# Performance work log

Measured on AMD Instinct MI355X. Metric: run time of the kernel, lower is better.

The kernel has to match this reference:

```python
import jax, jax.numpy as jnp
import numpy as np

B, D_IN, D_H, D_OUT, E = 4096, 1024, 4096, 1024, 8
N_ACTIVE = 5              # max(1, int(8 * 0.625))
TEMP = float(np.e)        # BoltzmannGate default temperature
N_CAMP_A = E // 2


def setup_inputs() -> dict:
    key = jax.random.key(0)
    ks = jax.random.split(key, 6)
    s_in = 1.0 / np.sqrt(D_IN)
    s_h = 1.0 / np.sqrt(D_H)
    return {
        "x": jax.random.normal(ks[0], (B, D_IN), jnp.float32),
        "gate_w": jax.random.normal(ks[1], (D_IN, E), jnp.float32) * s_in,
        "gate_b": jnp.zeros((E,), jnp.float32),
        "w1": jax.random.normal(ks[2], (E, D_IN, D_H), jnp.float32) * s_in,
        "b1": jnp.zeros((E, D_H), jnp.float32),
        "w2": jax.random.normal(ks[3], (E, D_H, D_OUT), jnp.float32) * s_h,
        "b2": jnp.zeros((E, D_OUT), jnp.float32),
        "ph_alpha": jnp.array(1.0, jnp.float32),
        "ph_beta": jnp.array(0.0, jnp.float32),
    }


def _forward(x, gate_w, gate_b, w1, b1, w2, b2, ph_alpha, ph_beta):
    # BoltzmannGate: softmax over temperature-scaled scores, top-k mask, renorm
    scores = (x @ gate_w + gate_b) / TEMP                 # [B, E]
    probs = jax.nn.softmax(scores, axis=-1)
    _, topk_idx = jax.lax.top_k(probs, N_ACTIVE)          # [B, k]
    rows = jnp.arange(x.shape[0])[:, None]
    mask = jnp.zeros_like(probs).at[rows, topk_idx].set(1.0)
    w = probs * mask
    weights = w / (w.sum(axis=-1, keepdims=True) + 1e-8)  # [B, E]

    # Dense evaluation of all experts (dropout is inference-mode identity)
    h = jax.nn.relu(jnp.einsum("bi,eih->beh", x, w1) + b1)     # [B, E, H]
    e_out = jnp.einsum("beh,eho->beo", h, w2) + b2             # [B, E, O]

    # Camp A = experts [0, E//2), Camp G = experts [E//2, E)
    out_a = jnp.einsum("be,beo->bo", weights[:, :N_CAMP_A], e_out[:, :N_CAMP_A])
    out_g = jnp.einsum("be,beo->bo", weights[:, N_CAMP_A:], e_out[:, N_CAMP_A:])

    repulsion = out_a - out_g
    # PH distance proxy computed on detached tensors in torch -> stop_gradient
    diff = jax.lax.stop_gradient(repulsion)
    l2 = jnp.linalg.norm(diff, axis=-1)                   # [B]
    var = jnp.var(diff, axis=-1)                          # population var, ddof=0
    ph_dist = l2 * (1.0 + var)
    ph_corr = jax.nn.sigmoid(ph_alpha * ph_dist + ph_beta) * 2.0  # in (0, 2)
    output = repulsion * ph_corr[:, None]
    return output, out_a, out_g


def reference(x, gate_w, gate_b, w1, b1, w2, b2, ph_alpha, ph_beta):
    return _forward(x, gate_w, gate_b, w1, b1, w2, b2, ph_alpha, ph_beta)
```

## Files before the change

### kernel.cpp

```cpp
#include <hip/hip_runtime.h>
#include <hip/hip_bf16.h>
#include <stdint.h>

typedef unsigned short u16;
typedef unsigned int u32;
typedef __attribute__((ext_vector_type(4))) float f32x4;
typedef __attribute__((ext_vector_type(4))) int i32x4;
typedef __attribute__((ext_vector_type(8))) u16 u16x8;
typedef __attribute__((ext_vector_type(8))) __bf16 bf16x8;

constexpr int BATCH = 4096, DIN = 1024, DH = 4096, DOUT = 1024, NEXP = 8;
constexpr int HS_CAP = 2816;

struct Ptr4 { float* p[4]; };

__device__ __forceinline__ u16 f2bf(float f) {
  u32 u = __float_as_uint(f);
  u += 0x7fffu + ((u >> 16) & 1u);
  return (u16)(u >> 16);
}

#define GLOAD_LDS16(gp, lp)                                                    \
  __builtin_amdgcn_global_load_lds(                                           \
      (__attribute__((address_space(1))) void*)(gp),                          \
      (__attribute__((address_space(3))) void*)(lp), 16, 0, 0)

#define BAR()                                                                  \
  { asm volatile("" ::: "memory"); __builtin_amdgcn_s_barrier();               \
    asm volatile("" ::: "memory"); }
#define VM4() asm volatile("s_waitcnt vmcnt(4)" ::: "memory")
#define VM0() asm volatile("s_waitcnt vmcnt(0)" ::: "memory")

#define STG4(q0, q1, kofs, dst)                                                \
  { GLOAD_LDS16((q0) + (kofs), (dst));                                         \
    GLOAD_LDS16((q1) + (kofs), (dst) + 4096); }

__global__ void gate_kernel(const float* __restrict__ x,
                            const float* __restrict__ gw,
                            const float* __restrict__ gb,
                            float* __restrict__ wgt) {
  const int wave = threadIdx.x >> 6, lane = threadIdx.x & 63;
  const int b = blockIdx.x * 4 + wave;
  const float* xr = x + (size_t)b * DIN;
  float acc[NEXP];
#pragma unroll
  for (int e = 0; e < NEXP; ++e) acc[e] = 0.f;
  for (int k = lane; k < DIN; k += 64) {
    const float xv = xr[k];
    const f32x4 g0 = *(const f32x4*)(gw + (size_t)k * NEXP);
    const f32x4 g1 = *(const f32x4*)(gw + (size_t)k * NEXP + 4);
    acc[0] += xv * g0[0]; acc[1] += xv * g0[1];
    acc[2] += xv * g0[2]; acc[3] += xv * g0[3];
    acc[4] += xv * g1[0]; acc[5] += xv * g1[1];
    acc[6] += xv * g1[2]; acc[7] += xv * g1[3];
  }
#pragma unroll
  for (int off = 32; off; off >>= 1)
#pragma unroll
    for (int e = 0; e < NEXP; ++e) acc[e] += __shfl_xor(acc[e], off);
  if (lane == 0) {
    const float invT = 0.36787944117144233f;
    float s[NEXP], mx = -1e30f;
    for (int e = 0; e < NEXP; ++e) { s[e] = (acc[e] + gb[e]) * invT; mx = fmaxf(mx, s[e]); }
    float p[NEXP], sum = 0.f;
    for (int e = 0; e < NEXP; ++e) { p[e] = expf(s[e] - mx); sum += p[e]; }
    const float inv = 1.f / sum;
    for (int e = 0; e < NEXP; ++e) p[e] *= inv;
    float w[NEXP], wsum = 0.f;
    for (int e = 0; e < NEXP; ++e) {
      int cnt = 0;
      for (int j = 0; j < NEXP; ++j) cnt += (p[j] > p[e]) || (p[j] == p[e] && j < e);
      w[e] = (cnt < 5) ? p[e] : 0.f;
      wsum += w[e];
    }
    const float inv2 = 1.f / (wsum + 1e-8f);
    for (int e = 0; e < NEXP; ++e) wgt[(size_t)b * NEXP + e] = w[e] * inv2;
  }
}

__global__ void assign_kernel(const float* __restrict__ wgt,
                              int* __restrict__ cnt, u16* __restrict__ ridx) {
  const int b = blockIdx.x * 256 + threadIdx.x;
#pragma unroll
  for (int e = 0; e < NEXP; ++e) {
    if (wgt[(size_t)b * NEXP + e] != 0.f) {
      const int pos = atomicAdd(&cnt[e], 1);
      if (pos < BATCH) ridx[e * BATCH + pos] = (u16)b;
    }
  }
}

__global__ void build_items(const int* __restrict__ cnt,
                            u32* __restrict__ items, int* __restrict__ itot) {
  if (threadIdx.x != 0) return;
  int t = 0;
  for (int e = 0; e < NEXP; ++e) {
    int c = cnt[e]; c = c < HS_CAP ? c : HS_CAP;
    const int nm = (c + 255) >> 8;
    for (int n = 0; n < DH / 256; ++n)
      for (int m = 0; m < nm; ++m)
        items[t++] = ((u32)e << 12) | ((u32)n << 6) | (u32)m;
  }
  itot[0] = t;
}

__global__ void gather_cvt(const float* __restrict__ x,
                           const int* __restrict__ cnt,
                           const u16* __restrict__ ridx,
                           u16* __restrict__ Xe) {
  const int e = blockIdx.y, p = blockIdx.x;
  int c = cnt[e]; c = c < HS_CAP ? c : HS_CAP;
  if (p >= c) return;
  const int row = ridx[e * BATCH + p];
  const float* s = x + (size_t)row * DIN;
  u16* d = Xe + ((size_t)e * HS_CAP + p) * DIN;
  const int t = threadIdx.x;
  const f32x4 a = *(const f32x4*)(s + t * 8);
  const f32x4 b = *(const f32x4*)(s + t * 8 + 4);
  u16x8 o;
  o[0] = f2bf(a[0]); o[1] = f2bf(a[1]); o[2] = f2bf(a[2]); o[3] = f2bf(a[3]);
  o[4] = f2bf(b[0]); o[5] = f2bf(b[1]); o[6] = f2bf(b[2]); o[7] = f2bf(b[3]);
  *(u16x8*)(d + t * 8) = o;
}

__global__ void transpose_cvt(const float* __restrict__ src, u16* __restrict__ dst,
                              int C, int ldd, size_t src_slice,
                              size_t dst_hi, size_t dst_lo) {
  __shared__ float ts[64][65];
  const int z = blockIdx.z;
  const float* s = src + (size_t)z * src_slice;
  u16* d = dst + (size_t)(z >> 2) * dst_hi + (size_t)(z & 3) * dst_lo;
  const int c0 = blockIdx.x * 64, r0 = blockIdx.y * 64;
  const int t = threadIdx.x;
  const int lr = t >> 4, lc = (t & 15) * 4;
#pragma unroll
  for (int i = 0; i < 4; ++i) {
    const f32x4 v = *(const f32x4*)(s + (size_t)(r0 + i * 16 + lr) * C + c0 + lc);
    ts[i * 16 + lr][lc] = v[0];
    ts[i * 16 + lr][lc + 1] = v[1];
    ts[i * 16 + lr][lc + 2] = v[2];
    ts[i * 16 + lr][lc + 3] = v[3];
  }
  __syncthreads();
  const int cc = t >> 3, r8 = (t & 7) * 8;
#pragma unroll
  for (int pass = 0; pass < 2; ++pass) {
    const int c = cc + pass * 32;
    u16x8 o;
#pragma unroll
    for (int j = 0; j < 8; ++j) o[j] = f2bf(ts[r8 + j][c]);
    *(u16x8*)(d + (size_t)(c0 + c) * ldd + r0 + r8) = o;
  }
}

__device__ __forceinline__ void rdB4(i32x4 rB[2][2], const char* base, int wc,
                                     int roff, int NH) {
#pragma unroll
  for (int n = 0; n < 2; ++n)
#pragma unroll
    for (int kk = 0; kk < 2; ++kk)
      rB[n][kk] = *(const i32x4*)(base + (((wc * 4 + NH * 2 + n) * 2 + kk) << 10) + roff);
}
template <int MH>
__device__ __forceinline__ void rdA8(i32x4 rA[4][2], const char* base, int wr, int roff) {
#pragma unroll
  for (int m = 0; m < 4; ++m)
#pragma unroll
    for (int kk = 0; kk < 2; ++kk)
      rA[m][kk] = *(const i32x4*)(base + (((wr * 8 + MH * 4 + m) * 2 + kk) << 10) + roff);
}
template <int MH, int NH>
__device__ __forceinline__ void mm16(f32x4 acc[8][4], const i32x4 rA[4][2],
                                     const i32x4 rB[2][2]) {
  __builtin_amdgcn_s_setprio(1);
#pragma unroll
  for (int m = 0; m < 4; ++m)
#pragma unroll
    for (int n = 0; n < 2; ++n)
#pragma unroll
      for (int kk = 0; kk < 2; ++kk)
        acc[MH * 4 + m][NH * 2 + n] = __builtin_amdgcn_mfma_f32_16x16x32_bf16(
            __builtin_bit_cast(bf16x8, rA[m][kk]),
            __builtin_bit_cast(bf16x8, rB[n][kk]),
            acc[MH * 4 + m][NH * 2 + n], 0, 0, 0);
  __builtin_amdgcn_s_setprio(0);
}

#define TILE_BODY(T, CA, CB_, DA_OT, DB_CB)                                    \
  {                                                                            \
    const int t_ = (T);                                                        \
    const bool g1 = (t_ + 1) < NT, g2 = (t_ + 2) < NT;                         \
    const int kA = (t_ + 1) * 64, kB = (t_ + 2) * 64;                          \
    rdA8<0>(rA, CA, wr, roff);                                                 \
    rdB4(rB0, CB_, wc, roff, 0);                                               \
    if (g1) STG4(qA0, qA1, kA, DA_OT);                                         \
    BAR();                                                                     \
    mm16<0, 0>(acc, rA, rB0);                                                  \
    BAR();                                                                     \
    rdB4(rB1, CB_, wc, roff, 1);                                               \
    if (g1) STG4(qA2, qA3, kA, DA_OT + 8192);                                  \
    BAR();                                                                     \
    mm16<0, 1>(acc, rA, rB1);                                                  \
    BAR();                                                                     \
    rdA8<1>(rA, CA, wr, roff);                                                 \
    if (g2) STG4(qB0, qB1, kB, DB_CB);                                         \
    BAR();                                                                     \
    mm16<1, 1>(acc, rA, rB1);                                                  \
    BAR();                                                                     \
    if (g2) {                                                                  \
      STG4(qB2, qB3, kB, DB_CB + 8192);                                        \
      BAR();                                                                   \
      mm16<1, 0>(acc, rA, rB0);                                                \
      VM4();                                                                   \
    } else {                                                                   \
      BAR();                                                                   \
      mm16<1, 0>(acc, rA, rB0);                                                \
      VM0();                                                                   \
    }                                                                          \
    BAR();                                                                     \
  }

__global__ __launch_bounds__(512, 2) void gemm256p(
    const u16* __restrict__ Xe, const u16* __restrict__ w1t,
    u16* __restrict__ Hs, const float* __restrict__ wgt,
    const float* __restrict__ b1,
    const int* __restrict__ cnt, const u16* __restrict__ ridx,
    const int* __restrict__ itot, const u32* __restrict__ items) {
  __shared__ __align__(16) u16 sA[2][16384];
  __shared__ __align__(16) u16 sB[2][16384];

  const int tid = threadIdx.x;
  const int w = tid >> 6, lane = tid & 63;
  const int l15 = lane & 15, lh = lane >> 4;
  const int wr = w >> 2, wc = w & 3;

  const int lp = lane ^ ((lane & 32) >> 4);
  const int grow = (w >> 1) * 16 + (lp >> 2);
  const int gcol = (w & 1) * 32 + (lp & 3) * 8;
  const int roff = l15 * 64 + ((lh * 16) ^ ((l15 & 8) << 2));
  const char* cA0 = (const char*)&sA[0][0];
  const char* cA1 = (const char*)&sA[1][0];
  const char* cB0 = (const char*)&sB[0][0];
  const char* cB1 = (const char*)&sB[1][0];
  u16* dA0 = &sA[0][w * 512];
  u16* dA1 = &sA[1][w * 512];
  u16* dB0 = &sB[0][w * 512];
  u16* dB1 = &sB[1][w * 512];

  const int total = itot[0];
  const int lo = (int)(((long)blockIdx.x * total) >> 8);
  const int hi = (int)((((long)blockIdx.x + 1) * total) >> 8);
  constexpr int NT = DIN / 64;

  for (int ii = lo; ii < hi; ++ii) {
    const u32 it = items[ii];
    const int e = it >> 12, n = (it >> 6) & 63, m = it & 63;
    const int bM = m * 256, bN = n * 256;
    int count = cnt[e]; count = count < HS_CAP ? count : HS_CAP;
    const int eoff = e * BATCH;

    const u16* A = Xe + (size_t)e * HS_CAP * DIN;
    const u16* Bt = w1t + (size_t)e * DH * DIN;
    const float* bias = b1 + (size_t)e * DH;
    u16* dstH = Hs + (size_t)e * HS_CAP * DH;

    const u16* qA0 = A + (size_t)(bM + grow) * DIN + gcol;
    const u16* qA1 = qA0 + (size_t)64 * DIN;
    const u16* qA2 = qA0 + (size_t)128 * DIN;
    const u16* qA3 = qA0 + (size_t)192 * DIN;
    const u16* qB0 = Bt + (size_t)(bN + grow) * DIN + gcol;
    const u16* qB1 = qB0 + (size_t)64 * DIN;
    const u16* qB2 = qB0 + (size_t)128 * DIN;
    const u16* qB3 = qB0 + (size_t)192 * DIN;

    f32x4 acc[8][4] = {};
    i32x4 rA[4][2], rB0[2][2], rB1[2][2];

    STG4(qB0, qB1, 0, dB0);
    STG4(qB2, qB3, 0, dB0 + 8192);
    STG4(qA0, qA1, 0, dA0);
    STG4(qA2, qA3, 0, dA0 + 8192);
    STG4(qB0, qB1, 64, dB1);
    STG4(qB2, qB3, 64, dB1 + 8192);
    VM4();
    BAR();

    for (int t = 0; t < NT; t += 2) {
      TILE_BODY(t, cA0, cB0, dA1, dB0);
      TILE_BODY(t + 1, cA1, cB1, dA0, dB1);
    }

#pragma unroll
    for (int m2 = 0; m2 < 8; ++m2)
#pragma unroll
      for (int r = 0; r < 4; ++r) {
        const int pos = bM + wr * 128 + m2 * 16 + lh * 4 + r;
        if (pos >= count) continue;
        const int orow = ridx[eoff + pos];
        const float wsc = wgt[(size_t)orow * NEXP + e];
#pragma unroll
        for (int nn = 0; nn < 4; ++nn) {
          const int col = bN + wc * 64 + nn * 16 + l15;
          float v = acc[m2][nn][r] + bias[col];
          v = fmaxf(v, 0.0f) * wsc;
          dstH[(size_t)pos * DH + col] = f2bf(v);
        }
      }
  }
}

template <int EPI>
__global__ __launch_bounds__(512, 2) void gemm256(
    const u16* __restrict__ A0, int lda,
    const u16* __restrict__ Bt0, int ldb, int K,
    u16* __restrict__ dstH0, Ptr4 parts,
    const float* __restrict__ wgt, const float* __restrict__ bias0,
    const int* __restrict__ cnt, const u16* __restrict__ ridx, int camp,
    int NM, int NN) {
  __shared__ __align__(16) u16 sA[2][16384];
  __shared__ __align__(16) u16 sB[2][16384];

  const int tid = threadIdx.x;
  const int w = tid >> 6, lane = tid & 63;
  const int l15 = lane & 15, lh = lane >> 4;
  const int wr = w >> 2, wc = w & 3;

  const int cpx = (int)gridDim.x >> 3;
  const int id = blockIdx.x;
  const int wk = (id & 7) * cpx + (id >> 3);
  const int m = wk % NM;
  const int n = (wk / NM) % NN;
  const int z = wk / (NM * NN);
  const int bM = m * 256, bN = n * 256;

  const int expert = camp * 4 + z;
  int count = cnt[expert];
  count = count < HS_CAP ? count : HS_CAP;
  if (bM >= count) return;
  const int eoff = expert * BATCH;

  const u16* A;
  const u16* Bt;
  const float* bias = bias0;
  u16* dstH = dstH0;
  if (EPI == 0) {
    A = A0 + (size_t)expert * HS_CAP * lda;
    Bt = Bt0 + (size_t)expert * DH * DIN;
    bias = bias0 + (size_t)expert * DH;
    dstH = dstH0 + (size_t)z * HS_CAP * DH;
  } else {
    A = A0 + (size_t)z * HS_CAP * lda;
    Bt = Bt0 + (size_t)z * DH;
  }

  const int lp = lane ^ ((lane & 32) >> 4);
  const int grow = (w >> 1) * 16 + (lp >> 2);
  const int gcol = (w & 1) * 32 + (lp & 3) * 8;

  const u16* qA0 = A + (size_t)(bM + grow) * lda + gcol;
  const u16* qA1 = qA0 + (size_t)64 * lda;
  const u16* qA2 = qA0 + (size_t)128 * lda;
  const u16* qA3 = qA0 + (size_t)192 * lda;
  const u16* qB0 = Bt + (size_t)(bN + grow) * ldb + gcol;
  const u16* qB1 = qB0 + (size_t)64 * ldb;
  const u16* qB2 = qB0 + (size_t)128 * ldb;
  const u16* qB3 = qB0 + (size_t)192 * ldb;

  u16* dA0 = &sA[0][w * 512];
  u16* dA1 = &sA[1][w * 512];
  u16* dB0 = &sB[0][w * 512];
  u16* dB1 = &sB[1][w * 512];

  const int roff = l15 * 64 + ((lh * 16) ^ ((l15 & 8) << 2));
  const char* cA0 = (const char*)&sA[0][0];
  const char* cA1 = (const char*)&sA[1][0];
  const char* cB0 = (const char*)&sB[0][0];
  const char* cB1 = (const char*)&sB[1][0];

  const int NT = K >> 6;
  f32x4 acc[8][4] = {};
  i32x4 rA[4][2], rB0[2][2], rB1[2][2];

  STG4(qB0, qB1, 0, dB0);
  STG4(qB2, qB3, 0, dB0 + 8192);
  STG4(qA0, qA1, 0, dA0);
  STG4(qA2, qA3, 0, dA0 + 8192);
  STG4(qB0, qB1, 64, dB1);
  STG4(qB2, qB3, 64, dB1 + 8192);
  VM4();
  BAR();

  for (int t = 0; t < NT; t += 2) {
    TILE_BODY(t, cA0, cB0, dA1, dB0);
    TILE_BODY(t + 1, cA1, cB1, dA0, dB1);
  }

  if (EPI == 0) {
#pragma unroll
    for (int m2 = 0; m2 < 8; ++m2)
#pragma unroll
      for (int r = 0; r < 4; ++r) {
        const int pos = bM + wr * 128 + m2 * 16 + lh * 4 + r;
        if (pos >= count) continue;
        const int orow = ridx[eoff + pos];
        const float wsc = wgt[(size_t)orow * NEXP + expert];
#pragma unroll
        for (int nn = 0; nn < 4; ++nn) {
          const int col = bN + wc * 64 + nn * 16 + l15;
          float v = acc[m2][nn][r] + bias[col];
          v = fmaxf(v, 0.0f) * wsc;
          dstH[(size_t)pos * DH + col] = f2bf(v);
        }
      }
  } else {
    float* __restrict__ P = parts.p[z];
#pragma unroll
    for (int m2 = 0; m2 < 8; ++m2)
#pragma unroll
      for (int r = 0; r < 4; ++r) {
        const int pos = bM + wr * 128 + m2 * 16 + lh * 4 + r;
        if (pos >= count) continue;
        const int orow = ridx[eoff + pos];
#pragma unroll
        for (int nn = 0; nn < 4; ++nn) {
          const int col = bN + wc * 64 + nn * 16 + l15;
          P[(size_t)orow * DOUT + col] = acc[m2][nn][r];
        }
      }
  }
}

__global__ void reduce_kernel(float* __restrict__ dst,
                              const float* __restrict__ p0, const float* __restrict__ p1,
                              const float* __restrict__ p2, const float* __restrict__ p3,
                              const float* __restrict__ wgt,
                              const float* __restrict__ b2c, int camp) {
  const int b = blockIdx.x, t = threadIdx.x;
  const f32x4 wv = *(const f32x4*)(wgt + (size_t)b * NEXP + camp * 4);
  const size_t ro = (size_t)b * DOUT;
#pragma unroll
  for (int j = 0; j < 4; ++j) {
    const int i = j * 256 + t;
    float acc = wv[0] * b2c[i] + wv[1] * b2c[DOUT + i] +
                wv[2] * b2c[2 * DOUT + i] + wv[3] * b2c[3 * DOUT + i];
    acc += (wv[0] != 0.f) ? p0[ro + i] : 0.f;
    acc += (wv[1] != 0.f) ? p1[ro + i] : 0.f;
    acc += (wv[2] != 0.f) ? p2[ro + i] : 0.f;
    acc += (wv[3] != 0.f) ? p3[ro + i] : 0.f;
    dst[ro + i] = acc;
  }
}

__global__ void final_kernel(float* __restrict__ out,
                             const float* __restrict__ alpha,
                             const float* __restrict__ beta) {
  const int b = blockIdx.x, t = threadIdx.x;
  const float* pa = out + (size_t)BATCH * DOUT + (size_t)b * DOUT;
  const float* pg = out + (size_t)2 * BATCH * DOUT + (size_t)b * DOUT;
  float* po = out + (size_t)b * DOUT;
  float d[4], s1 = 0.f, s2 = 0.f;
#pragma unroll
  for (int j = 0; j < 4; ++j) {
    const int i = j * 256 + t;
    d[j] = pa[i] - pg[i];
    s1 += d[j];
    s2 += d[j] * d[j];
  }
#pragma unroll
  for (int off = 32; off; off >>= 1) {
    s1 += __shfl_xor(s1, off);
    s2 += __shfl_xor(s2, off);
  }
  __shared__ float r1[4], r2[4];
  if ((t & 63) == 0) { r1[t >> 6] = s1; r2[t >> 6] = s2; }
  __syncthreads();
  s1 = r1[0] + r1[1] + r1[2] + r1[3];
  s2 = r2[0] + r2[1] + r2[2] + r2[3];
  const float mean = s1 * (1.f / DOUT);
  const float var = s2 * (1.f / DOUT) - mean * mean;
  const float dist = sqrtf(s2) * (1.f + var);
  const float zz = alpha[0] * dist + beta[0];
  const float corr = 2.f / (1.f + expf(-zz));
#pragma unroll
  for (int j = 0; j < 4; ++j) po[j * 256 + t] = d[j] * corr;
}

extern "C" void kernel_launch(void* const* d_in, const int* in_sizes, int n_in,
                              void* d_out, int out_size, void* d_ws, size_t ws_size,
                              hipStream_t stream) {
  const float* x   = (const float*)d_in[0];
  const float* gw  = (const float*)d_in[1];
  const float* gb  = (const float*)d_in[2];
  const float* w1  = (const float*)d_in[3];
  const float* b1  = (const float*)d_in[4];
  const float* w2  = (const float*)d_in[5];
  const float* b2  = (const float*)d_in[6];
  const float* pha = (const float*)d_in[7];
  const float* phb = (const float*)d_in[8];
  float* out = (float*)d_out;
  float* out_a = out + (size_t)BATCH * DOUT;
  float* out_g = out + (size_t)2 * BATCH * DOUT;

  char* ws = (char*)d_ws;
  float* wgt  = (float*)ws;
  int* cnt    = (int*)(ws + 131072);
  u16* ridx   = (u16*)(ws + 135168);
  u32* items  = (u32*)(ws + 200704);
  int* itot   = (int*)(ws + 258048);
  u16* Xe     = (u16*)(ws + 262144);
  constexpr size_t XE_BYTES  = (size_t)NEXP * HS_CAP * DIN * 2;
  constexpr size_t W1T_BYTES = (size_t)NEXP * DH * DIN * 2;
  constexpr size_t W2T_BYTES = (size_t)DOUT * 4 * DH * 2;
  constexpr size_t P_BYTES   = (size_t)BATCH * DOUT * 4;
  constexpr size_t HS_E      = (size_t)HS_CAP * DH * 2;
  const size_t w1t_off = 262144 + XE_BYTES;
  u16* w1t = (u16*)(ws + w1t_off);

  const size_t merged_need = w1t_off + W1T_BYTES + 2 * P_BYTES + 8 * HS_E;
  const bool merged = (ws_size >= merged_need);

  constexpr int NM = HS_CAP / 256;
  constexpr int NN1 = DH / 256, NN2 = DOUT / 256;

  gate_kernel<<<BATCH / 4, 256, 0, stream>>>(x, gw, gb, wgt);
  hipMemsetAsync(cnt, 0, NEXP * sizeof(int), stream);
  assign_kernel<<<BATCH / 256, 256, 0, stream>>>(wgt, cnt, ridx);
  build_items<<<1, 64, 0, stream>>>(cnt, items, itot);
  gather_cvt<<<dim3(HS_CAP, NEXP), 128, 0, stream>>>(x, cnt, ridx, Xe);
  transpose_cvt<<<dim3(DH / 64, DIN / 64, NEXP), 256, 0, stream>>>(
      w1, w1t, DH, DIN, (size_t)DIN * DH, (size_t)4 * DH * DIN, (size_t)DH * DIN);

  if (merged) {
    float* P0 = (float*)(ws + w1t_off + W1T_BYTES);
    float* P1 = (float*)(ws + w1t_off + W1T_BYTES + P_BYTES);
    u16* Hs   = (u16*)(ws + w1t_off + W1T_BYTES + 2 * P_BYTES);
    u16* w2t0 = w1t;
    u16* w2t1 = (u16*)((char*)w1t + W2T_BYTES);
    Ptr4 pc0 = {{out_a, out, out_g, P0}};
    Ptr4 pc1 = {{out_g, out, P0, P1}};

    gemm256p<<<256, 512, 0, stream>>>(Xe, w1t, Hs, wgt, b1, cnt, ridx, itot, items);
    transpose_cvt<<<dim3(DOUT / 64, DH / 64, 4), 256, 0, stream>>>(
        w2, w2t0, DOUT, 4 * DH, (size_t)DH * DOUT, 0, (size_t)DH);
    transpose_cvt<<<dim3(DOUT / 64, DH / 64, 4), 256, 0, stream>>>(
        w2 + (size_t)4 * DH * DOUT, w2t1, DOUT, 4 * DH, (size_t)DH * DOUT, 0, (size_t)DH);

    gemm256<2><<<NM * NN2 * 4, 512, 0, stream>>>(
        Hs, DH, w2t0, 4 * DH, DH, nullptr, pc0, nullptr, nullptr, cnt, ridx, 0, NM, NN2);
    reduce_kernel<<<BATCH, 256, 0, stream>>>(out_a, out_a, out, out_g, P0, wgt, b2, 0);
    gemm256<2><<<NM * NN2 * 4, 512, 0, stream>>>(
        Hs + (size_t)4 * HS_CAP * DH, DH, w2t1, 4 * DH, DH, nullptr, pc1,
        nullptr, nullptr, cnt, ridx, 1, NM, NN2);
    reduce_kernel<<<BATCH, 256, 0, stream>>>(out_g, out_g, out, P0, P1, wgt,
                                             b2 + (size_t)4 * DOUT, 1);
  } else {
    u16* w2t1 = w1t;
    u16* w2t0 = (u16*)(ws + w1t_off + W1T_BYTES);
    float* P0 = (float*)(ws + w1t_off + W1T_BYTES + W2T_BYTES);
    float* P1 = (float*)(ws + w1t_off + W1T_BYTES + W2T_BYTES + P_BYTES);
    u16* Hs   = (u16*)(ws + w1t_off + W1T_BYTES + W2T_BYTES + 2 * P_BYTES);
    Ptr4 pc0 = {{out_a, out, out_g, P0}};
    Ptr4 pc1 = {{out_g, out, P0, P1}};

    transpose_cvt<<<dim3(DOUT / 64, DH / 64, 4), 256, 0, stream>>>(
        w2, w2t0, DOUT, 4 * DH, (size_t)DH * DOUT, 0, (size_t)DH);
    gemm256<0><<<NM * NN1 * 4, 512, 0, stream>>>(
        Xe, DIN, w1t, DIN, DIN, Hs, pc0, wgt, b1, cnt, ridx, 0, NM, NN1);
    transpose_cvt<<<dim3(DOUT / 64, DH / 64, 4), 256, 0, stream>>>(
        w2 + (size_t)4 * DH * DOUT, w2t1, DOUT, 4 * DH, (size_t)DH * DOUT, 0, (size_t)DH);
    gemm256<2><<<NM * NN2 * 4, 512, 0, stream>>>(
        Hs, DH, w2t0, 4 * DH, DH, nullptr, pc0, nullptr, nullptr, cnt, ridx, 0, NM, NN2);
    reduce_kernel<<<BATCH, 256, 0, stream>>>(out_a, out_a, out, out_g, P0, wgt, b2, 0);
    gemm256<0><<<NM * NN1 * 4, 512, 0, stream>>>(
        Xe, DIN, w1t, DIN, DIN, Hs, pc1, wgt, b1, cnt, ridx, 1, NM, NN1);
    gemm256<2><<<NM * NN2 * 4, 512, 0, stream>>>(
        Hs, DH, w2t1, 4 * DH, DH, nullptr, pc1, nullptr, nullptr, cnt, ridx, 1, NM, NN2);
    reduce_kernel<<<BATCH, 256, 0, stream>>>(out_g, out_g, out, P0, P1, wgt,
                                             b2 + (size_t)4 * DOUT, 1);
  }

  final_kernel<<<BATCH, 256, 0, stream>>>(out, pha, phb);
}
```

Measured before the change: 728.3 us.

## Overlap camp-A layer-2 GEMM with camp-G layer-1 GEMM in one combo launch

Removes the persistent item-list GEMM and its build_items kernel. When the workspace is large enough, w2 is transposed into separate buffers up front. The camp-A layer-1 GEMM then runs, followed by a single combined launch whose blocks run either the camp-A layer-2 GEMM or the camp-G layer-1 GEMM, so the two overlap on the device. The last reduce is also fused into the final PH-correction kernel, removing one pass over the output. The cost is a larger workspace requirement and a heterogeneous grid whose tiles may be unevenly balanced.

```diff
diff --git a/kernel.cpp b/kernel.cpp
--- a/kernel.cpp
+++ b/kernel.cpp
@@ -88,20 +88,6 @@
       if (pos < BATCH) ridx[e * BATCH + pos] = (u16)b;
     }
   }
-}
-
-__global__ void build_items(const int* __restrict__ cnt,
-                            u32* __restrict__ items, int* __restrict__ itot) {
-  if (threadIdx.x != 0) return;
-  int t = 0;
-  for (int e = 0; e < NEXP; ++e) {
-    int c = cnt[e]; c = c < HS_CAP ? c : HS_CAP;
-    const int nm = (c + 255) >> 8;
-    for (int n = 0; n < DH / 256; ++n)
-      for (int m = 0; m < nm; ++m)
-        items[t++] = ((u32)e << 12) | ((u32)n << 6) | (u32)m;
-  }
-  itot[0] = t;
 }
 
 __global__ void gather_cvt(const float* __restrict__ x,
@@ -220,95 +206,6 @@
     BAR();                                                                     \
   }
 
-__global__ __launch_bounds__(512, 2) void gemm256p(
-    const u16* __restrict__ Xe, const u16* __restrict__ w1t,
-    u16* __restrict__ Hs, const float* __restrict__ wgt,
-    const float* __restrict__ b1,
-    const int* __restrict__ cnt, const u16* __restrict__ ridx,
-    const int* __restrict__ itot, const u32* __restrict__ items) {
-  __shared__ __align__(16) u16 sA[2][16384];
-  __shared__ __align__(16) u16 sB[2][16384];
-
-  const int tid = threadIdx.x;
-  const int w = tid >> 6, lane = tid & 63;
-  const int l15 = lane & 15, lh = lane >> 4;
-  const int wr = w >> 2, wc = w & 3;
-
-  const int lp = lane ^ ((lane & 32) >> 4);
-  const int grow = (w >> 1) * 16 + (lp >> 2);
-  const int gcol = (w & 1) * 32 + (lp & 3) * 8;
-  const int roff = l15 * 64 + ((lh * 16) ^ ((l15 & 8) << 2));
-  const char* cA0 = (const char*)&sA[0][0];
-  const char* cA1 = (const char*)&sA[1][0];
-  const char* cB0 = (const char*)&sB[0][0];
-  const char* cB1 = (const char*)&sB[1][0];
-  u16* dA0 = &sA[0][w * 512];
-  u16* dA1 = &sA[1][w * 512];
-  u16* dB0 = &sB[0][w * 512];
-  u16* dB1 = &sB[1][w * 512];
-
-  const int total = itot[0];
-  const int lo = (int)(((long)blockIdx.x * total) >> 8);
-  const int hi = (int)((((long)blockIdx.x + 1) * total) >> 8);
-  constexpr int NT = DIN / 64;
-
-  for (int ii = lo; ii < hi; ++ii) {
-    const u32 it = items[ii];
-    const int e = it >> 12, n = (it >> 6) & 63, m = it & 63;
-    const int bM = m * 256, bN = n * 256;
-    int count = cnt[e]; count = count < HS_CAP ? count : HS_CAP;
-    const int eoff = e * BATCH;
-
-    const u16* A = Xe + (size_t)e * HS_CAP * DIN;
-    const u16* Bt = w1t + (size_t)e * DH * DIN;
-    const float* bias = b1 + (size_t)e * DH;
-    u16* dstH = Hs + (size_t)e * HS_CAP * DH;
-
-    const u16* qA0 = A + (size_t)(bM + grow) * DIN + gcol;
-    const u16* qA1 = qA0 + (size_t)64 * DIN;
-    const u16* qA2 = qA0 + (size_t)128 * DIN;
-    const u16* qA3 = qA0 + (size_t)192 * DIN;
-    const u16* qB0 = Bt + (size_t)(bN + grow) * DIN + gcol;
-    const u16* qB1 = qB0 + (size_t)64 * DIN;
-    const u16* qB2 = qB0 + (size_t)128 * DIN;
-    const u16* qB3 = qB0 + (size_t)192 * DIN;
-
-    f32x4 acc[8][4] = {};
-    i32x4 rA[4][2], rB0[2][2], rB1[2][2];
-
-    STG4(qB0, qB1, 0, dB0);
-    STG4(qB2, qB3, 0, dB0 + 8192);
-    STG4(qA0, qA1, 0, dA0);
-    STG4(qA2, qA3, 0, dA0 + 8192);
-    STG4(qB0, qB1, 64, dB1);
-    STG4(qB2, qB3, 64, dB1 + 8192);
-    VM4();
-    BAR();
-
-    for (int t = 0; t < NT; t += 2) {
-      TILE_BODY(t, cA0, cB0, dA1, dB0);
-      TILE_BODY(t + 1, cA1, cB1, dA0, dB1);
-    }
-
-#pragma unroll
-    for (int m2 = 0; m2 < 8; ++m2)
-#pragma unroll
-      for (int r = 0; r < 4; ++r) {
-        const int pos = bM + wr * 128 + m2 * 16 + lh * 4 + r;
-        if (pos >= count) continue;
-        const int orow = ridx[eoff + pos];
-        const float wsc = wgt[(size_t)orow * NEXP + e];
-#pragma unroll
-        for (int nn = 0; nn < 4; ++nn) {
-          const int col = bN + wc * 64 + nn * 16 + l15;
-          float v = acc[m2][nn][r] + bias[col];
-          v = fmaxf(v, 0.0f) * wsc;
-          dstH[(size_t)pos * DH + col] = f2bf(v);
-        }
-      }
-  }
-}
-
 template <int EPI>
 __global__ __launch_bounds__(512, 2) void gemm256(
     const u16* __restrict__ A0, int lda,
@@ -430,6 +327,131 @@
   }
 }
 
+__global__ __launch_bounds__(512, 2) void gemm_combo(
+    const u16* __restrict__ Hs0, const u16* __restrict__ w2t0, Ptr4 pc0,
+    const u16* __restrict__ Xe, const u16* __restrict__ w1t,
+    u16* __restrict__ HsW, const float* __restrict__ b1,
+    const float* __restrict__ wgt,
+    const int* __restrict__ cnt, const u16* __restrict__ ridx, int l2n) {
+  __shared__ __align__(16) u16 sA[2][16384];
+  __shared__ __align__(16) u16 sB[2][16384];
+
+  const int tid = threadIdx.x;
+  const int w = tid >> 6, lane = tid & 63;
+  const int l15 = lane & 15, lh = lane >> 4;
+  const int wr = w >> 2, wc = w & 3;
+
+  const bool isL2 = (int)blockIdx.x < l2n;
+  const int id = isL2 ? (int)blockIdx.x : (int)blockIdx.x - l2n;
+  const int tot = isL2 ? l2n : ((int)gridDim.x - l2n);
+  const int cpx = tot >> 3;
+  const int wk = (id & 7) * cpx + (id >> 3);
+  const int NM = HS_CAP / 256;
+  const int NN = isL2 ? (DOUT / 256) : (DH / 256);
+  const int m = wk % NM;
+  const int n = (wk / NM) % NN;
+  const int z = wk / (NM * NN);
+  const int bM = m * 256, bN = n * 256;
+
+  const int expert = isL2 ? z : 4 + z;
+  int count = cnt[expert];
+  count = count < HS_CAP ? count : HS_CAP;
+  if (bM >= count) return;
+  const int eoff = expert * BATCH;
+
+  const u16* A; const u16* Bt;
+  int lda, ldb, K;
+  const float* bias = nullptr;
+  u16* dstH = nullptr;
+  if (isL2) {
+    A = Hs0 + (size_t)z * HS_CAP * DH;  lda = DH;
+    Bt = w2t0 + (size_t)z * DH;         ldb = 4 * DH;
+    K = DH;
+  } else {
+    A = Xe + (size_t)expert * HS_CAP * DIN;  lda = DIN;
+    Bt = w1t + (size_t)expert * DH * DIN;    ldb = DIN;
+    K = DIN;
+    bias = b1 + (size_t)expert * DH;
+    dstH = HsW + (size_t)expert * HS_CAP * DH;
+  }
+
+  const int lp = lane ^ ((lane & 32) >> 4);
+  const int grow = (w >> 1) * 16 + (lp >> 2);
+  const int gcol = (w & 1) * 32 + (lp & 3) * 8;
+
+  const u16* qA0 = A + (size_t)(bM + grow) * lda + gcol;
+  const u16* qA1 = qA0 + (size_t)64 * lda;
+  const u16* qA2 = qA0 + (size_t)128 * lda;
+  const u16* qA3 = qA0 + (size_t)192 * lda;
+  const u16* qB0 = Bt + (size_t)(bN + grow) * ldb + gcol;
+  const u16* qB1 = qB0 + (size_t)64 * ldb;
+  const u16* qB2 = qB0 + (size_t)128 * ldb;
+  const u16* qB3 = qB0 + (size_t)192 * ldb;
+
+  u16* dA0 = &sA[0][w * 512];
+  u16* dA1 = &sA[1][w * 512];
+  u16* dB0 = &sB[0][w * 512];
+  u16* dB1 = &sB[1][w * 512];
+
+  const int roff = l15 * 64 + ((lh * 16) ^ ((l15 & 8) << 2));
+  const char* cA0 = (const char*)&sA[0][0];
+  const char* cA1 = (const char*)&sA[1][0];
+  const char* cB0 = (const char*)&sB[0][0];
+  const char* cB1 = (const char*)&sB[1][0];
+
+  const int NT = K >> 6;
+  f32x4 acc[8][4] = {};
+  i32x4 rA[4][2], rB0[2][2], rB1[2][2];
+
+  STG4(qB0, qB1, 0, dB0);
+  STG4(qB2, qB3, 0, dB0 + 8192);
+  STG4(qA0, qA1, 0, dA0);
+  STG4(qA2, qA3, 0, dA0 + 8192);
+  STG4(qB0, qB1, 64, dB1);
+  STG4(qB2, qB3, 64, dB1 + 8192);
+  VM4();
+  BAR();
+
+  for (int t = 0; t < NT; t += 2) {
+    TILE_BODY(t, cA0, cB0, dA1, dB0);
+    TILE_BODY(t + 1, cA1, cB1, dA0, dB1);
+  }
+
+  if (isL2) {
+    float* __restrict__ P = pc0.p[z];
+#pragma unroll
+    for (int m2 = 0; m2 < 8; ++m2)
+#pragma unroll
+      for (int r = 0; r < 4; ++r) {
+        const int pos = bM + wr * 128 + m2 * 16 + lh * 4 + r;
+        if (pos >= count) continue;
+        const int orow = ridx[eoff + pos];
+#pragma unroll
+        for (int nn = 0; nn < 4; ++nn) {
+          const int col = bN + wc * 64 + nn * 16 + l15;
+          P[(size_t)orow * DOUT + col] = acc[m2][nn][r];
+        }
+      }
+  } else {
+#pragma unroll
+    for (int m2 = 0; m2 < 8; ++m2)
+#pragma unroll
+      for (int r = 0; r < 4; ++r) {
+        const int pos = bM + wr * 128 + m2 * 16 + lh * 4 + r;
+        if (pos >= count) continue;
+        const int orow = ridx[eoff + pos];
+        const float wsc = wgt[(size_t)orow * NEXP + expert];
+#pragma unroll
+        for (int nn = 0; nn < 4; ++nn) {
+          const int col = bN + wc * 64 + nn * 16 + l15;
+          float v = acc[m2][nn][r] + bias[col];
+          v = fmaxf(v, 0.0f) * wsc;
+          dstH[(size_t)pos * DH + col] = f2bf(v);
+        }
+      }
+  }
+}
+
 __global__ void reduce_kernel(float* __restrict__ dst,
                               const float* __restrict__ p0, const float* __restrict__ p1,
                               const float* __restrict__ p2, const float* __restrict__ p3,
@@ -451,18 +473,33 @@
   }
 }
 
-__global__ void final_kernel(float* __restrict__ out,
-                             const float* __restrict__ alpha,
-                             const float* __restrict__ beta) {
+__global__ void reduce_final_kernel(float* __restrict__ out,
+                                    const float* __restrict__ p0,
+                                    const float* __restrict__ p1,
+                                    const float* __restrict__ p2,
+                                    const float* __restrict__ p3,
+                                    const float* __restrict__ wgt,
+                                    const float* __restrict__ b2c,
+                                    const float* __restrict__ alpha,
+                                    const float* __restrict__ beta) {
   const int b = blockIdx.x, t = threadIdx.x;
-  const float* pa = out + (size_t)BATCH * DOUT + (size_t)b * DOUT;
-  const float* pg = out + (size_t)2 * BATCH * DOUT + (size_t)b * DOUT;
-  float* po = out + (size_t)b * DOUT;
-  float d[4], s1 = 0.f, s2 = 0.f;
+  const f32x4 wv = *(const f32x4*)(wgt + (size_t)b * NEXP + 4);
+  const size_t ro = (size_t)b * DOUT;
+  const float* pa = out + (size_t)BATCH * DOUT + ro;
+  float* pg = out + (size_t)2 * BATCH * DOUT + ro;
+  float* po = out + ro;
+  float g[4], d[4], s1 = 0.f, s2 = 0.f;
 #pragma unroll
   for (int j = 0; j < 4; ++j) {
     const int i = j * 256 + t;
-    d[j] = pa[i] - pg[i];
+    float acc = wv[0] * b2c[i] + wv[1] * b2c[DOUT + i] +
+                wv[2] * b2c[2 * DOUT + i] + wv[3] * b2c[3 * DOUT + i];
+    acc += (wv[0] != 0.f) ? p0[ro + i] : 0.f;
+    acc += (wv[1] != 0.f) ? p1[ro + i] : 0.f;
+    acc += (wv[2] != 0.f) ? p2[ro + i] : 0.f;
+    acc += (wv[3] != 0.f) ? p3[ro + i] : 0.f;
+    g[j] = acc;
+    d[j] = pa[i] - acc;
     s1 += d[j];
     s2 += d[j] * d[j];
   }
@@ -482,7 +519,11 @@
   const float zz = alpha[0] * dist + beta[0];
   const float corr = 2.f / (1.f + expf(-zz));
 #pragma unroll
-  for (int j = 0; j < 4; ++j) po[j * 256 + t] = d[j] * corr;
+  for (int j = 0; j < 4; ++j) {
+    const int i = j * 256 + t;
+    pg[i] = g[j];
+    po[i] = d[j] * corr;
+  }
 }
 
 extern "C" void kernel_launch(void* const* d_in, const int* in_sizes, int n_in,
@@ -505,8 +546,6 @@
   float* wgt  = (float*)ws;
   int* cnt    = (int*)(ws + 131072);
   u16* ridx   = (u16*)(ws + 135168);
-  u32* items  = (u32*)(ws + 200704);
-  int* itot   = (int*)(ws + 258048);
   u16* Xe     = (u16*)(ws + 262144);
   constexpr size_t XE_BYTES  = (size_t)NEXP * HS_CAP * DIN * 2;
   constexpr size_t W1T_BYTES = (size_t)NEXP * DH * DIN * 2;
@@ -516,8 +555,8 @@
   const size_t w1t_off = 262144 + XE_BYTES;
   u16* w1t = (u16*)(ws + w1t_off);
 
+  const size_t pipe_need = w1t_off + W1T_BYTES + 2 * W2T_BYTES + 2 * P_BYTES + 8 * HS_E;
   const size_t merged_need = w1t_off + W1T_BYTES + 2 * P_BYTES + 8 * HS_E;
-  const bool merged = (ws_size >= merged_need);
 
   constexpr int NM = HS_CAP / 256;
   constexpr int NN1 = DH / 256, NN2 = DOUT / 256;
@@ -525,12 +564,36 @@
   gate_kernel<<<BATCH / 4, 256, 0, stream>>>(x, gw, gb, wgt);
   hipMemsetAsync(cnt, 0, NEXP * sizeof(int), stream);
   assign_kernel<<<BATCH / 256, 256, 0, stream>>>(wgt, cnt, ridx);
-  build_items<<<1, 64, 0, stream>>>(cnt, items, itot);
   gather_cvt<<<dim3(HS_CAP, NEXP), 128, 0, stream>>>(x, cnt, ridx, Xe);
   transpose_cvt<<<dim3(DH / 64, DIN / 64, NEXP), 256, 0, stream>>>(
       w1, w1t, DH, DIN, (size_t)DIN * DH, (size_t)4 * DH * DIN, (size_t)DH * DIN);
 
-  if (merged) {
+  if (ws_size >= pipe_need) {
+    u16* w2t0 = (u16*)(ws + w1t_off + W1T_BYTES);
+    u16* w2t1 = (u16*)(ws + w1t_off + W1T_BYTES + W2T_BYTES);
+    float* P0 = (float*)(ws + w1t_off + W1T_BYTES + 2 * W2T_BYTES);
+    float* P1 = (float*)(ws + w1t_off + W1T_BYTES + 2 * W2T_BYTES + P_BYTES);
+    u16* Hs   = (u16*)(ws + w1t_off + W1T_BYTES + 2 * W2T_BYTES + 2 * P_BYTES);
+    Ptr4 pc0 = {{out_a, out, out_g, P0}};
+    Ptr4 pc1 = {{out_g, out, P0, P1}};
+
+    transpose_cvt<<<dim3(DOUT / 64, DH / 64, 4), 256, 0, stream>>>(
+        w2, w2t0, DOUT, 4 * DH, (size_t)DH * DOUT, 0, (size_t)DH);
+    transpose_cvt<<<dim3(DOUT / 64, DH / 64, 4), 256, 0, stream>>>(
+        w2 + (size_t)4 * DH * DOUT, w2t1, DOUT, 4 * DH, (size_t)DH * DOUT, 0, (size_t)DH);
+
+    gemm256<0><<<NM * NN1 * 4, 512, 0, stream>>>(
+        Xe, DIN, w1t, DIN, DIN, Hs, pc0, wgt, b1, cnt, ridx, 0, NM, NN1);
+    gemm_combo<<<NM * NN2 * 4 + NM * NN1 * 4, 512, 0, stream>>>(
+        Hs, w2t0, pc0, Xe, w1t, Hs, b1, wgt, cnt, ridx, NM * NN2 * 4);
+    reduce_kernel<<<BATCH, 256, 0, stream>>>(out_a, out_a, out, out_g, P0, wgt, b2, 0);
+    gemm256<2><<<NM * NN2 * 4, 512, 0, stream>>>(
+        Hs + (size_t)4 * HS_CAP * DH, DH, w2t1, 4 * DH, DH, nullptr, pc1,
+        nullptr, nullptr, cnt, ridx, 1, NM, NN2);
+    reduce_final_kernel<<<BATCH, 256, 0, stream>>>(out, out_g, out, P0, P1,
+                                                   wgt, b2 + (size_t)4 * DOUT,
+                                                   pha, phb);
+  } else if (ws_size >= merged_need) {
     float* P0 = (float*)(ws + w1t_off + W1T_BYTES);
     float* P1 = (float*)(ws + w1t_off + W1T_BYTES + P_BYTES);
     u16* Hs   = (u16*)(ws + w1t_off + W1T_BYTES + 2 * P_BYTES);
@@ -539,20 +602,21 @@
     Ptr4 pc0 = {{out_a, out, out_g, P0}};
     Ptr4 pc1 = {{out_g, out, P0, P1}};
 
-    gemm256p<<<256, 512, 0, stream>>>(Xe, w1t, Hs, wgt, b1, cnt, ridx, itot, items);
+    gemm256<0><<<NM * NN1 * 8, 512, 0, stream>>>(
+        Xe, DIN, w1t, DIN, DIN, Hs, pc0, wgt, b1, cnt, ridx, 0, NM, NN1);
     transpose_cvt<<<dim3(DOUT / 64, DH / 64, 4), 256, 0, stream>>>(
         w2, w2t0, DOUT, 4 * DH, (size_t)DH * DOUT, 0, (size_t)DH);
     transpose_cvt<<<dim3(DOUT / 64, DH / 64, 4), 256, 0, stream>>>(
         w2 + (size_t)4 * DH * DOUT, w2t1, DOUT, 4 * DH, (size_t)DH * DOUT, 0, (size_t)DH);
-
     gemm256<2><<<NM * NN2 * 4, 512, 0, stream>>>(
         Hs, DH, w2t0, 4 * DH, DH, nullptr, pc0, nullptr, nullptr, cnt, ridx, 0, NM, NN2);
     reduce_kernel<<<BATCH, 256, 0, stream>>>(out_a, out_a, out, out_g, P0, wgt, b2, 0);
     gemm256<2><<<NM * NN2 * 4, 512, 0, stream>>>(
         Hs + (size_t)4 * HS_CAP * DH, DH, w2t1, 4 * DH, DH, nullptr, pc1,
         nullptr, nullptr, cnt, ridx, 1, NM, NN2);
-    reduce_kernel<<<BATCH, 256, 0, stream>>>(out_g, out_g, out, P0, P1, wgt,
-                                             b2 + (size_t)4 * DOUT, 1);
+    reduce_final_kernel<<<BATCH, 256, 0, stream>>>(out, out_g, out, P0, P1,
+                                                   wgt, b2 + (size_t)4 * DOUT,
+                                                   pha, phb);
   } else {
     u16* w2t1 = w1t;
     u16* w2t0 = (u16*)(ws + w1t_off + W1T_BYTES);
@@ -575,9 +639,8 @@
         Xe, DIN, w1t, DIN, DIN, Hs, pc1, wgt, b1, cnt, ridx, 1, NM, NN1);
     gemm256<2><<<NM * NN2 * 4, 512, 0, stream>>>(
         Hs, DH, w2t1, 4 * DH, DH, nullptr, pc1, nullptr, nullptr, cnt, ridx, 1, NM, NN2);
-    reduce_kernel<<<BATCH, 256, 0, stream>>>(out_g, out_g, out, P0, P1, wgt,
-                                             b2 + (size_t)4 * DOUT, 1);
-  }
-
-  final_kernel<<<BATCH, 256, 0, stream>>>(out, pha, phb);
-}
+    reduce_final_kernel<<<BATCH, 256, 0, stream>>>(out, out_g, out, P0, P1,
+                                                   wgt, b2 + (size_t)4 * DOUT,
+                                                   pha, phb);
+  }
+}
```

Result: faster. 650.8 us (-10.6%).
